# Optimization experiments

Hardware: AMD Instinct MI355X
Metric: run time of the kernel (lower is better)

Reference implementation:

```python
import jax, jax.numpy as jnp
import numpy as np

N = 50000      # nodes
E = 800000     # edges
F = 128        # num_features
DIM = 128      # dim
NF = 4         # n_factor
ND = DIM // NF # n_dim = 32
NL = 3         # n_layer
NC = 10        # n_class
G = 256        # num graphs in batch


def setup_inputs() -> dict:
    key = jax.random.key(0)
    ks = jax.random.split(key, 20)
    w = lambda k, shape, fan: (jax.random.normal(k, shape, jnp.float32) / np.sqrt(fan)).astype(jnp.float32)
    inp = {}
    inp["x"] = jax.random.normal(ks[0], (N, F), jnp.float32)
    inp["edge_index"] = jax.random.randint(ks[1], (2, E), 0, N)
    inp["batch"] = jnp.sort(jax.random.randint(ks[2], (N,), 0, G))
    # attention branch: lin0 (F->DIM) and att linear (2*DIM -> 1) per factor
    inp["lin0_W"] = w(ks[3], (NF, F, DIM), F)
    inp["lin0_b"] = jnp.zeros((NF, DIM), jnp.float32)
    inp["att_W"] = w(ks[4], (NF, 2 * DIM), 2 * DIM)
    inp["att_b"] = jnp.zeros((NF,), jnp.float32)
    # encoder per-factor input linear (F -> ND)
    inp["enc_W"] = w(ks[5], (NF, F, ND), F)
    inp["enc_b"] = jnp.zeros((NF, ND), jnp.float32)
    # GraphConv per factor/layer: lin_rel (with bias) + lin_root (no bias)
    inp["conv_Wrel"] = w(ks[6], (NF, NL, ND, ND), ND)
    inp["conv_brel"] = jnp.zeros((NF, NL, ND), jnp.float32)
    inp["conv_Wroot"] = w(ks[7], (NF, NL, ND, ND), ND)
    # GRU per factor (input ND, hidden ND), torch layout: [3*H, in]
    inp["gru_Wih"] = w(ks[8], (NF, 3 * ND, ND), ND)
    inp["gru_Whh"] = w(ks[9], (NF, 3 * ND, ND), ND)
    inp["gru_bih"] = jnp.zeros((NF, 3 * ND), jnp.float32)
    inp["gru_bhh"] = jnp.zeros((NF, 3 * ND), jnp.float32)
    # head
    inp["fc1_W"] = w(ks[10], (DIM, DIM), DIM)
    inp["fc1_b"] = jnp.zeros((DIM,), jnp.float32)
    inp["fc2_W"] = w(ks[11], (DIM, NC), DIM)
    inp["fc2_b"] = jnp.zeros((NC,), jnp.float32)
    return inp


def _gru_step(m, h, Wih, Whh, bih, bhh):
    # torch GRUCell math; gates order [r, z, n]
    gi = m @ Wih.T + bih   # [N, 3H]
    gh = h @ Whh.T + bhh
    ir, iz, inn = jnp.split(gi, 3, axis=-1)
    hr, hz, hn = jnp.split(gh, 3, axis=-1)
    r = jax.nn.sigmoid(ir + hr)
    z = jax.nn.sigmoid(iz + hz)
    n = jnp.tanh(inn + r * hn)
    return (1.0 - z) * n + z * h


def reference(x, edge_index, batch, lin0_W, lin0_b, att_W, att_b, enc_W, enc_b,
              conv_Wrel, conv_brel, conv_Wroot, gru_Wih, gru_Whh, gru_bih, gru_bhh,
              fc1_W, fc1_b, fc2_W, fc2_b):
    src, dst = edge_index[0], edge_index[1]
    counts = jnp.maximum(jax.ops.segment_sum(jnp.ones((N,), jnp.float32), batch, num_segments=G), 1.0)
    outs, atts = [], []
    for f in range(NF):
        # edge attention: sigmoid(6 * Linear([lin0(x[src]) || lin0(x[dst])]))
        a = x @ lin0_W[f] + lin0_b[f]                     # [N, DIM]
        Wl, Wr = att_W[f, :DIM], att_W[f, DIM:]
        e = a[src] @ Wl + a[dst] @ Wr + att_b[f]          # [E]
        att_i = jax.nn.sigmoid(6.0 * e)
        atts.append(att_i)
        # disentangled encoder for this factor
        out = x @ enc_W[f] + enc_b[f]                     # [N, ND]
        h = out
        for l in range(NL):
            # GraphConv: lin_rel(scatter_add(x[src]*w -> dst)) + lin_root(x)
            msg = out[src] * att_i[:, None]               # [E, ND]
            agg = jax.ops.segment_sum(msg, dst, num_segments=N)
            m = jax.nn.relu(agg @ conv_Wrel[f, l] + conv_brel[f, l] + out @ conv_Wroot[f, l])
            h = _gru_step(m, h, gru_Wih[f], gru_Whh[f], gru_bih[f], gru_bhh[f])
            out = h
        pooled = jax.ops.segment_sum(out, batch, num_segments=G) / counts[:, None]  # [G, ND]
        outs.append(pooled)
    out_cat = jnp.concatenate(outs, axis=-1)              # [G, DIM]
    pred = jax.nn.relu(out_cat @ fc1_W + fc1_b) @ fc2_W + fc2_b  # [G, NC]
    return pred, jnp.stack(atts, 0), jnp.stack(outs, 0)
```

## Files before the change

kernel.cpp:

```cpp
#include <hip/hip_runtime.h>
#include <hip/hip_fp16.h>
#include <math.h>

#define N   50000
#define E   800000
#define F   128
#define DIM 128
#define NF  4
#define ND  32
#define NL  3
#define NC  10
#define G   256
#define NB  196

typedef __attribute__((ext_vector_type(8))) short  s16x8;
typedef __attribute__((ext_vector_type(4))) float  f32x4;

__device__ __forceinline__ float sigm(float v) { return 1.0f / (1.0f + __expf(-v)); }

__device__ __forceinline__ unsigned int f2bf(float x) {
    unsigned int u = __float_as_uint(x);
    return (u + 0x7FFFu + ((u >> 16) & 1u)) >> 16;
}

__device__ __forceinline__ void split8(const float* v, s16x8& hi, s16x8& lo) {
    #pragma unroll
    for (int i = 0; i < 8; ++i) {
        float x = v[i];
        unsigned int h = f2bf(x);
        float hf = __uint_as_float(h << 16);
        hi[i] = (short)h;
        lo[i] = (short)f2bf(x - hf);
    }
}

#define MFMA(a, b, c) c = __builtin_amdgcn_mfma_f32_16x16x32_bf16(a, b, c, 0, 0, 0)
#define MF3(xh, xl, wh, wl, c) do { MFMA(xh, wh, c); MFMA(xh, wl, c); MFMA(xl, wh, c); } while (0)

__global__ void prep_kernel(const float* __restrict__ lin0_W, const float* __restrict__ lin0_b,
                            const float* __restrict__ att_W, const float* __restrict__ att_b,
                            float* __restrict__ vl, float* __restrict__ vr, float* __restrict__ cc) {
    int t = blockIdx.x * blockDim.x + threadIdx.x;
    if (t < NF * F) {
        int f = t >> 7, k = t & 127;
        const float* W  = lin0_W + (size_t)f * F * DIM + (size_t)k * DIM;
        const float* wl = att_W + f * 2 * DIM;
        const float* wr = wl + DIM;
        float sl = 0.f, sr = 0.f;
        for (int j = 0; j < DIM; ++j) { sl += W[j] * wl[j]; sr += W[j] * wr[j]; }
        vl[t] = sl; vr[t] = sr;
    }
    if (t < NF) {
        const float* b  = lin0_b + t * DIM;
        const float* wl = att_W + t * 2 * DIM;
        const float* wr = wl + DIM;
        float s = att_b[t];
        for (int j = 0; j < DIM; ++j) s += b[j] * (wl[j] + wr[j]);
        cc[t] = s;
    }
}

__global__ void wfrag_kernel(const float* __restrict__ Wrel, const float* __restrict__ Wroot,
                             const float* __restrict__ Wih, const float* __restrict__ Whh,
                             const float* __restrict__ enc_W,
                             const float* __restrict__ vl, const float* __restrict__ vr,
                             unsigned short* __restrict__ convfrag,
                             unsigned short* __restrict__ grufrag,
                             unsigned short* __restrict__ encfrag,
                             unsigned short* __restrict__ attfrag) {
    int b = blockIdx.x;
    int l = threadIdx.x;
    int lr = l & 15, lg = l >> 4;
    if (b < 12) {
        const float* wrelg  = Wrel  + (size_t)b * 1024;
        const float* wrootg = Wroot + (size_t)b * 1024;
        #pragma unroll
        for (int H = 0; H < 2; ++H) {
            #pragma unroll
            for (int i = 0; i < 8; ++i) {
                float x = wrelg[(lg * 8 + i) * 32 + H * 16 + lr];
                unsigned int h = f2bf(x);
                convfrag[(((size_t)b * 8 + 0 + H) * 64 + l) * 8 + i] = (unsigned short)h;
                convfrag[(((size_t)b * 8 + 2 + H) * 64 + l) * 8 + i] =
                    (unsigned short)f2bf(x - __uint_as_float(h << 16));
                x = wrootg[(lg * 8 + i) * 32 + H * 16 + lr];
                h = f2bf(x);
                convfrag[(((size_t)b * 8 + 4 + H) * 64 + l) * 8 + i] = (unsigned short)h;
                convfrag[(((size_t)b * 8 + 6 + H) * 64 + l) * 8 + i] =
                    (unsigned short)f2bf(x - __uint_as_float(h << 16));
            }
        }
    } else if (b < 16) {
        int f = b - 12;
        const float* wihg = Wih + (size_t)f * 3072;
        const float* whhg = Whh + (size_t)f * 3072;
        #pragma unroll
        for (int m = 0; m < 6; ++m) {
            const float* base = (m < 3 ? wihg : whhg) + (size_t)((m % 3) * 32) * 32;
            #pragma unroll
            for (int H = 0; H < 2; ++H) {
                int col = H * 16 + lr;
                #pragma unroll
                for (int i = 0; i < 8; ++i) {
                    float x = base[(size_t)col * 32 + lg * 8 + i];
                    unsigned int h = f2bf(x);
                    grufrag[(((size_t)(f * 6 + m) * 4 + H) * 64 + l) * 8 + i] = (unsigned short)h;
                    grufrag[(((size_t)(f * 6 + m) * 4 + 2 + H) * 64 + l) * 8 + i] =
                        (unsigned short)f2bf(x - __uint_as_float(h << 16));
                }
            }
        }
    } else {
        int f = b - 16;
        const float* we = enc_W + (size_t)f * F * ND;
        #pragma unroll
        for (int c = 0; c < 4; ++c) {
            #pragma unroll
            for (int i = 0; i < 8; ++i) {
                int k = c * 32 + lg * 8 + i;
                #pragma unroll
                for (int H = 0; H < 2; ++H) {
                    float x = we[(size_t)k * 32 + H * 16 + lr];
                    unsigned int h = f2bf(x);
                    encfrag[((((size_t)(f * 4 + c) * 2 + H) * 2 + 0) * 64 + l) * 8 + i] =
                        (unsigned short)h;
                    encfrag[((((size_t)(f * 4 + c) * 2 + H) * 2 + 1) * 64 + l) * 8 + i] =
                        (unsigned short)f2bf(x - __uint_as_float(h << 16));
                }
                float av = (lr == 0) ? vl[f * F + k] : (lr == 1) ? vr[f * F + k] : 0.f;
                unsigned int ha = f2bf(av);
                attfrag[(((size_t)(f * 4 + c) * 2 + 0) * 64 + l) * 8 + i] = (unsigned short)ha;
                attfrag[(((size_t)(f * 4 + c) * 2 + 1) * 64 + l) * 8 + i] =
                    (unsigned short)f2bf(av - __uint_as_float(ha << 16));
            }
        }
    }
}

__global__ __launch_bounds__(256) void encode_kernel(
        const float* __restrict__ x,
        const unsigned short* __restrict__ encfrag,
        const unsigned short* __restrict__ attfrag,
        const float* __restrict__ enc_b,
        float* __restrict__ out, unsigned short* __restrict__ st16,
        float* __restrict__ alr) {
    int tid = threadIdx.x;
    int f  = __builtin_amdgcn_readfirstlane(tid >> 6);
    int l  = tid & 63;
    int lr = l & 15, lg = l >> 4;
    int node0 = blockIdx.x * 32;

    s16x8 beh[4][2], bel[4][2], bah[4], bal[4];
    #pragma unroll
    for (int c = 0; c < 4; ++c) {
        #pragma unroll
        for (int H = 0; H < 2; ++H) {
            beh[c][H] = *(const s16x8*)&encfrag[((((size_t)(f*4 + c)*2 + H)*2 + 0)*64 + l)*8];
            bel[c][H] = *(const s16x8*)&encfrag[((((size_t)(f*4 + c)*2 + H)*2 + 1)*64 + l)*8];
        }
        bah[c] = *(const s16x8*)&attfrag[(((size_t)(f*4 + c)*2 + 0)*64 + l)*8];
        bal[c] = *(const s16x8*)&attfrag[(((size_t)(f*4 + c)*2 + 1)*64 + l)*8];
    }
    float be0 = enc_b[f*32 + lr], be1 = enc_b[f*32 + 16 + lr];

    #pragma unroll
    for (int s = 0; s < 2; ++s) {
        int n0 = node0 + s * 16;
        int na = n0 + lr; int nac = na < N ? na : N - 1;
        const float* px = x + (size_t)nac * F + lg * 8;
        s16x8 xh[4], xl[4];
        #pragma unroll
        for (int c = 0; c < 4; ++c) {
            float v[8];
            float4 q0 = *(const float4*)(px + c * 32);
            float4 q1 = *(const float4*)(px + c * 32 + 4);
            v[0]=q0.x; v[1]=q0.y; v[2]=q0.z; v[3]=q0.w; v[4]=q1.x; v[5]=q1.y; v[6]=q1.z; v[7]=q1.w;
            split8(v, xh[c], xl[c]);
        }
        f32x4 o0 = {be0, be0, be0, be0};
        f32x4 o1 = {be1, be1, be1, be1};
        f32x4 ca = {0.f, 0.f, 0.f, 0.f};
        #pragma unroll
        for (int c = 0; c < 4; ++c) {
            MF3(xh[c], xl[c], beh[c][0], bel[c][0], o0);
            MF3(xh[c], xl[c], beh[c][1], bel[c][1], o1);
            MF3(xh[c], xl[c], bah[c],    bal[c],    ca);
        }
        #pragma unroll
        for (int j = 0; j < 4; ++j) {
            int n = n0 + lg * 4 + j;
            if (n < N) {
                out[(size_t)n * DIM + f * ND + lr]       = o0[j];
                out[(size_t)n * DIM + f * ND + 16 + lr]  = o1[j];
                st16[(size_t)n * DIM + f * ND + lr]      = (unsigned short)f2bf(o0[j]);
                st16[(size_t)n * DIM + f * ND + 16 + lr] = (unsigned short)f2bf(o1[j]);
                if (lr == 0)      alr[(size_t)n * 8 + f]     = ca[j];
                else if (lr == 1) alr[(size_t)n * 8 + 4 + f] = ca[j];
            }
        }
    }
}

__global__ void hist_kernel(const int* __restrict__ ei, int* __restrict__ deg) {
    int e = blockIdx.x * 256 + threadIdx.x;
    if (e < E) atomicAdd(&deg[ei[E + e]], 1);
}

__global__ void scan1_kernel(const int* __restrict__ deg, int* __restrict__ rowp,
                             int* __restrict__ bsum) {
    __shared__ int sh[256];
    int i = blockIdx.x * 256 + threadIdx.x;
    int v = (i < N) ? deg[i] : 0;
    sh[threadIdx.x] = v;
    __syncthreads();
    for (int off = 1; off < 256; off <<= 1) {
        int t = 0;
        if ((int)threadIdx.x >= off) t = sh[threadIdx.x - off];
        __syncthreads();
        sh[threadIdx.x] += t;
        __syncthreads();
    }
    if (i < N) rowp[i] = sh[threadIdx.x] - v;
    if (threadIdx.x == 255) bsum[blockIdx.x] = sh[255];
}

__global__ void scan2_kernel(int* __restrict__ bsum) {
    __shared__ int sh[256];
    int v = ((int)threadIdx.x < NB) ? bsum[threadIdx.x] : 0;
    sh[threadIdx.x] = v;
    __syncthreads();
    for (int off = 1; off < 256; off <<= 1) {
        int t = 0;
        if ((int)threadIdx.x >= off) t = sh[threadIdx.x - off];
        __syncthreads();
        sh[threadIdx.x] += t;
        __syncthreads();
    }
    if ((int)threadIdx.x < NB) bsum[threadIdx.x] = sh[threadIdx.x] - v;
}

__global__ void scan3_kernel(int* __restrict__ rowp, const int* __restrict__ bsum) {
    int i = blockIdx.x * 256 + threadIdx.x;
    if (i < N) rowp[i] += bsum[i >> 8];
}

__global__ void fill_kernel(const int* __restrict__ ei, const float* __restrict__ alr,
                            const float* __restrict__ cc,
                            const int* __restrict__ rowp, int* __restrict__ cnt,
                            uint4* __restrict__ erec, float* __restrict__ atts) {
    int e = blockIdx.x * 256 + threadIdx.x;
    if (e >= E) return;
    int s = ei[e];
    int d = ei[E + e];
    float4 al = *(const float4*)(alr + (size_t)s * 8);
    float4 ar = *(const float4*)(alr + (size_t)d * 8 + 4);
    float a0 = sigm(6.f * (al.x + ar.x + cc[0]));
    float a1 = sigm(6.f * (al.y + ar.y + cc[1]));
    float a2 = sigm(6.f * (al.z + ar.z + cc[2]));
    float a3 = sigm(6.f * (al.w + ar.w + cc[3]));
    atts[e]                 = a0;
    atts[(size_t)E + e]     = a1;
    atts[2 * (size_t)E + e] = a2;
    atts[3 * (size_t)E + e] = a3;
    unsigned int p01 = (unsigned int)__half_as_ushort(__float2half(a0))
                     | ((unsigned int)__half_as_ushort(__float2half(a1)) << 16);
    unsigned int p23 = (unsigned int)__half_as_ushort(__float2half(a2))
                     | ((unsigned int)__half_as_ushort(__float2half(a3)) << 16);
    int slot = rowp[d] + atomicAdd(&cnt[d], 1);
    erec[slot] = make_uint4((unsigned int)s, p01, p23, 0u);
}

__global__ __launch_bounds__(256) void gather_kernel(
        const uint4* __restrict__ erec,
        const int* __restrict__ rowp, const int* __restrict__ deg,
        const unsigned short* __restrict__ st16,
        unsigned int* __restrict__ agghi, unsigned int* __restrict__ agglo) {
    int gw = (blockIdx.x << 2) | ((int)threadIdx.x >> 6);
    int n = __builtin_amdgcn_readfirstlane(gw);
    int lane = threadIdx.x & 63;
    int f = lane >> 4;
    int beg = rowp[n];
    int cnt = deg[n];
    const unsigned char* rp = (const unsigned char*)(erec + beg);
    const int aoff = 4 + (f >> 1) * 4;
    const int ash  = (f & 1) * 16;
    const unsigned short* ob = st16 + lane * 2;
    float ax = 0.f, ay = 0.f;
    int i = 0;
    #define RECS(k)  (*(const int*)(rp + (size_t)(i + k) * 16))
    #define RECA(k)  __half2float(__ushort_as_half((unsigned short)( \
                        (*(const unsigned int*)(rp + (size_t)(i + k) * 16 + aoff)) >> ash)))
    for (; i + 8 <= cnt; i += 8) {
        int s0 = RECS(0), s1 = RECS(1), s2 = RECS(2), s3 = RECS(3);
        int s4 = RECS(4), s5 = RECS(5), s6 = RECS(6), s7 = RECS(7);
        float a0 = RECA(0), a1 = RECA(1), a2 = RECA(2), a3 = RECA(3);
        float a4 = RECA(4), a5 = RECA(5), a6 = RECA(6), a7 = RECA(7);
        unsigned int u0 = *(const unsigned int*)(ob + (size_t)s0 * DIM);
        unsigned int u1 = *(const unsigned int*)(ob + (size_t)s1 * DIM);
        unsigned int u2 = *(const unsigned int*)(ob + (size_t)s2 * DIM);
        unsigned int u3 = *(const unsigned int*)(ob + (size_t)s3 * DIM);
        unsigned int u4 = *(const unsigned int*)(ob + (size_t)s4 * DIM);
        unsigned int u5 = *(const unsigned int*)(ob + (size_t)s5 * DIM);
        unsigned int u6 = *(const unsigned int*)(ob + (size_t)s6 * DIM);
        unsigned int u7 = *(const unsigned int*)(ob + (size_t)s7 * DIM);
        ax += a0 * __uint_as_float(u0 << 16) + a1 * __uint_as_float(u1 << 16)
            + a2 * __uint_as_float(u2 << 16) + a3 * __uint_as_float(u3 << 16)
            + a4 * __uint_as_float(u4 << 16) + a5 * __uint_as_float(u5 << 16)
            + a6 * __uint_as_float(u6 << 16) + a7 * __uint_as_float(u7 << 16);
        ay += a0 * __uint_as_float(u0 & 0xFFFF0000u) + a1 * __uint_as_float(u1 & 0xFFFF0000u)
            + a2 * __uint_as_float(u2 & 0xFFFF0000u) + a3 * __uint_as_float(u3 & 0xFFFF0000u)
            + a4 * __uint_as_float(u4 & 0xFFFF0000u) + a5 * __uint_as_float(u5 & 0xFFFF0000u)
            + a6 * __uint_as_float(u6 & 0xFFFF0000u) + a7 * __uint_as_float(u7 & 0xFFFF0000u);
    }
    for (; i + 4 <= cnt; i += 4) {
        int s0 = RECS(0), s1 = RECS(1), s2 = RECS(2), s3 = RECS(3);
        float a0 = RECA(0), a1 = RECA(1), a2 = RECA(2), a3 = RECA(3);
        unsigned int u0 = *(const unsigned int*)(ob + (size_t)s0 * DIM);
        unsigned int u1 = *(const unsigned int*)(ob + (size_t)s1 * DIM);
        unsigned int u2 = *(const unsigned int*)(ob + (size_t)s2 * DIM);
        unsigned int u3 = *(const unsigned int*)(ob + (size_t)s3 * DIM);
        ax += a0 * __uint_as_float(u0 << 16) + a1 * __uint_as_float(u1 << 16)
            + a2 * __uint_as_float(u2 << 16) + a3 * __uint_as_float(u3 << 16);
        ay += a0 * __uint_as_float(u0 & 0xFFFF0000u) + a1 * __uint_as_float(u1 & 0xFFFF0000u)
            + a2 * __uint_as_float(u2 & 0xFFFF0000u) + a3 * __uint_as_float(u3 & 0xFFFF0000u);
    }
    for (; i < cnt; ++i) {
        int s = RECS(0);
        float a = RECA(0);
        unsigned int u = *(const unsigned int*)(ob + (size_t)s * DIM);
        ax += a * __uint_as_float(u << 16);
        ay += a * __uint_as_float(u & 0xFFFF0000u);
    }
    #undef RECS
    #undef RECA
    unsigned int hx = f2bf(ax), hy = f2bf(ay);
    float fx = __uint_as_float(hx << 16), fy = __uint_as_float(hy << 16);
    agghi[(size_t)n * 64 + lane] = hx | (hy << 16);
    agglo[(size_t)n * 64 + lane] = f2bf(ax - fx) | (f2bf(ay - fy) << 16);
}

__global__ __launch_bounds__(256) void update_kernel(
        const unsigned int* __restrict__ agghi, const unsigned int* __restrict__ agglo,
        float* __restrict__ out, unsigned short* __restrict__ st16,
        const unsigned short* __restrict__ convfrag, const unsigned short* __restrict__ grufrag,
        const float* __restrict__ brel,
        const float* __restrict__ bih, const float* __restrict__ bhh, int lay) {
    __shared__ __align__(16) unsigned short mls[NF][2][2][16 * 40];
    int tid = threadIdx.x;
    int f   = __builtin_amdgcn_readfirstlane(tid >> 6);
    int l   = tid & 63;
    int lr  = l & 15;
    int lg  = l >> 4;
    int node0 = blockIdx.x * 32;

    const unsigned short* cf = convfrag + (size_t)(f * NL + lay) * 8 * 64 * 8;
    s16x8 wrelh[2], wrell[2], wrooth[2], wrootl[2];
    #pragma unroll
    for (int H = 0; H < 2; ++H) {
        wrelh[H]  = *(const s16x8*)&cf[((0 + H) * 64 + l) * 8];
        wrell[H]  = *(const s16x8*)&cf[((2 + H) * 64 + l) * 8];
        wrooth[H] = *(const s16x8*)&cf[((4 + H) * 64 + l) * 8];
        wrootl[H] = *(const s16x8*)&cf[((6 + H) * 64 + l) * 8];
    }
    const unsigned short* gf = grufrag + (size_t)f * 6 * 4 * 64 * 8;
    s16x8 wirh[2], wirl[2], wizh[2], wizl[2], winh[2], winl[2];
    s16x8 whrh[2], whrl[2], whzh[2], whzl[2], whnh[2], whnl[2];
    #pragma unroll
    for (int H = 0; H < 2; ++H) {
        wirh[H] = *(const s16x8*)&gf[((0 * 4 + H) * 64 + l) * 8];
        wirl[H] = *(const s16x8*)&gf[((0 * 4 + 2 + H) * 64 + l) * 8];
        wizh[H] = *(const s16x8*)&gf[((1 * 4 + H) * 64 + l) * 8];
        wizl[H] = *(const s16x8*)&gf[((1 * 4 + 2 + H) * 64 + l) * 8];
        winh[H] = *(const s16x8*)&gf[((2 * 4 + H) * 64 + l) * 8];
        winl[H] = *(const s16x8*)&gf[((2 * 4 + 2 + H) * 64 + l) * 8];
        whrh[H] = *(const s16x8*)&gf[((3 * 4 + H) * 64 + l) * 8];
        whrl[H] = *(const s16x8*)&gf[((3 * 4 + 2 + H) * 64 + l) * 8];
        whzh[H] = *(const s16x8*)&gf[((4 * 4 + H) * 64 + l) * 8];
        whzl[H] = *(const s16x8*)&gf[((4 * 4 + 2 + H) * 64 + l) * 8];
        whnh[H] = *(const s16x8*)&gf[((5 * 4 + H) * 64 + l) * 8];
        whnl[H] = *(const s16x8*)&gf[((5 * 4 + 2 + H) * 64 + l) * 8];
    }

    float br_[2], bir_[2], biz_[2], bin_[2], bhn_[2];
    #pragma unroll
    for (int H = 0; H < 2; ++H) {
        int c = H * 16 + lr;
        br_[H]  = brel[(f * NL + lay) * 32 + c];
        bir_[H] = bih[f * 96 + c]      + bhh[f * 96 + c];
        biz_[H] = bih[f * 96 + 32 + c] + bhh[f * 96 + 32 + c];
        bin_[H] = bih[f * 96 + 64 + c];
        bhn_[H] = bhh[f * 96 + 64 + c];
    }

    const unsigned short* ahp = (const unsigned short*)agghi;
    const unsigned short* alp = (const unsigned short*)agglo;

    #pragma unroll
    for (int s = 0; s < 2; ++s) {
        int n0 = node0 + s * 16;
        unsigned short* mHi = &mls[f][s][0][0];
        unsigned short* mLo = &mls[f][s][1][0];
        int na  = n0 + lr;
        int nac = na < N ? na : N - 1;
        s16x8 aggH = *(const s16x8*)&ahp[(size_t)nac * DIM + f * ND + lg * 8];
        s16x8 aggL = *(const s16x8*)&alp[(size_t)nac * DIM + f * ND + lg * 8];
        const float* ph = out + (size_t)nac * DIM + f * ND + lg * 8;
        float vh[8];
        { float4 q0 = *(const float4*)ph, q1 = *(const float4*)(ph + 4);
          vh[0]=q0.x; vh[1]=q0.y; vh[2]=q0.z; vh[3]=q0.w; vh[4]=q1.x; vh[5]=q1.y; vh[6]=q1.z; vh[7]=q1.w; }
        s16x8 hH, hL;
        split8(vh, hH, hL);
        float hj0[4], hj1[4];
        #pragma unroll
        for (int j = 0; j < 4; ++j) {
            int nn_ = n0 + lg * 4 + j;
            int nnc = nn_ < N ? nn_ : N - 1;
            hj0[j] = out[(size_t)nnc * DIM + f * ND + lr];
            hj1[j] = out[(size_t)nnc * DIM + f * ND + 16 + lr];
        }

        f32x4 c0 = {br_[0], br_[0], br_[0], br_[0]};
        f32x4 c1 = {br_[1], br_[1], br_[1], br_[1]};
        MF3(aggH, aggL, wrelh[0],  wrell[0],  c0);
        MF3(hH,   hL,   wrooth[0], wrootl[0], c0);
        MF3(aggH, aggL, wrelh[1],  wrell[1],  c1);
        MF3(hH,   hL,   wrooth[1], wrootl[1], c1);

        #pragma unroll
        for (int j = 0; j < 4; ++j) {
            int row = lg * 4 + j;
            float v0 = fmaxf(c0[j], 0.f);
            float v1 = fmaxf(c1[j], 0.f);
            unsigned int h0 = f2bf(v0);
            unsigned int h1 = f2bf(v1);
            mHi[row * 40 + lr]      = (unsigned short)h0;
            mHi[row * 40 + 16 + lr] = (unsigned short)h1;
            mLo[row * 40 + lr]      = (unsigned short)f2bf(v0 - __uint_as_float(h0 << 16));
            mLo[row * 40 + 16 + lr] = (unsigned short)f2bf(v1 - __uint_as_float(h1 << 16));
        }
        __asm__ volatile("s_waitcnt lgkmcnt(0)" ::: "memory");
        __builtin_amdgcn_sched_barrier(0x37);
        s16x8 mH = *(const s16x8*)&mHi[lr * 40 + lg * 8];
        s16x8 mL = *(const s16x8*)&mLo[lr * 40 + lg * 8];

        f32x4 gr0 = {bir_[0], bir_[0], bir_[0], bir_[0]};
        f32x4 gr1 = {bir_[1], bir_[1], bir_[1], bir_[1]};
        f32x4 gz0 = {biz_[0], biz_[0], biz_[0], biz_[0]};
        f32x4 gz1 = {biz_[1], biz_[1], biz_[1], biz_[1]};
        f32x4 gn0 = {bin_[0], bin_[0], bin_[0], bin_[0]};
        f32x4 gn1 = {bin_[1], bin_[1], bin_[1], bin_[1]};
        f32x4 gh0 = {bhn_[0], bhn_[0], bhn_[0], bhn_[0]};
        f32x4 gh1 = {bhn_[1], bhn_[1], bhn_[1], bhn_[1]};
        MF3(mH, mL, wirh[0], wirl[0], gr0);  MF3(hH, hL, whrh[0], whrl[0], gr0);
        MF3(mH, mL, wirh[1], wirl[1], gr1);  MF3(hH, hL, whrh[1], whrl[1], gr1);
        MF3(mH, mL, wizh[0], wizl[0], gz0);  MF3(hH, hL, whzh[0], whzl[0], gz0);
        MF3(mH, mL, wizh[1], wizl[1], gz1);  MF3(hH, hL, whzh[1], whzl[1], gz1);
        MF3(mH, mL, winh[0], winl[0], gn0);
        MF3(mH, mL, winh[1], winl[1], gn1);
        MF3(hH, hL, whnh[0], whnl[0], gh0);
        MF3(hH, hL, whnh[1], whnl[1], gh1);

        #pragma unroll
        for (int j = 0; j < 4; ++j) {
            int n = n0 + lg * 4 + j;
            float r0 = sigm(gr0[j]);
            float z0 = sigm(gz0[j]);
            float t0 = 2.f * sigm(2.f * (gn0[j] + r0 * gh0[j])) - 1.f;
            float res0 = (1.f - z0) * t0 + z0 * hj0[j];
            float r1 = sigm(gr1[j]);
            float z1 = sigm(gz1[j]);
            float t1 = 2.f * sigm(2.f * (gn1[j] + r1 * gh1[j])) - 1.f;
            float res1 = (1.f - z1) * t1 + z1 * hj1[j];
            if (n < N) {
                out[(size_t)n * DIM + f * ND + lr]       = res0;
                out[(size_t)n * DIM + f * ND + 16 + lr]  = res1;
                st16[(size_t)n * DIM + f * ND + lr]      = (unsigned short)f2bf(res0);
                st16[(size_t)n * DIM + f * ND + 16 + lr] = (unsigned short)f2bf(res1);
            }
        }
    }
}

__global__ void goff_kernel(const int* __restrict__ batch, int* __restrict__ goff) {
    int g = threadIdx.x;
    int lo = 0, hi = N;
    while (lo < hi) {
        int mid = (lo + hi) >> 1;
        if (batch[mid] < g) lo = mid + 1; else hi = mid;
    }
    goff[g] = lo;
    if (g == 0) goff[G] = N;
}

__global__ void pool_kernel(const float* __restrict__ st, const int* __restrict__ goff,
                            float* __restrict__ pooled, float* __restrict__ outsout) {
    __shared__ float acc2[128];
    int g = blockIdx.x;
    int c = threadIdx.x & 127;
    int half = threadIdx.x >> 7;
    int beg = goff[g], cnt = goff[g + 1] - beg;
    float acc = 0.f;
    for (int i = half; i < cnt; i += 2) acc += st[(size_t)(beg + i) * DIM + c];
    if (half == 1) acc2[c] = acc;
    __syncthreads();
    if (half == 0) {
        float tot = acc + acc2[c];
        float val = tot / fmaxf((float)cnt, 1.0f);
        pooled[g * DIM + c] = val;
        int f = c >> 5, d = c & 31;
        outsout[((size_t)f * G + g) * ND + d] = val;
    }
}

__global__ void mlp_kernel(const float* __restrict__ pooled,
                           const float* __restrict__ fc1_W, const float* __restrict__ fc1_b,
                           const float* __restrict__ fc2_W, const float* __restrict__ fc2_b,
                           float* __restrict__ pred) {
    __shared__ float row[DIM], hid[DIM];
    int g = blockIdx.x, c = threadIdx.x;
    row[c] = pooled[(size_t)g * DIM + c];
    __syncthreads();
    float acc = fc1_b[c];
    #pragma unroll 8
    for (int k = 0; k < DIM; ++k) acc += row[k] * fc1_W[k * DIM + c];
    hid[c] = fmaxf(acc, 0.f);
    __syncthreads();
    if (c < NC) {
        float p = fc2_b[c];
        for (int k = 0; k < DIM; ++k) p += hid[k] * fc2_W[k * NC + c];
        pred[(size_t)g * NC + c] = p;
    }
}

extern "C" void kernel_launch(void* const* d_in, const int* in_sizes, int n_in,
                              void* d_out, int out_size, void* d_ws, size_t ws_size,
                              hipStream_t stream) {
    const float* x         = (const float*)d_in[0];
    const int*   ei        = (const int*)  d_in[1];
    const int*   batch     = (const int*)  d_in[2];
    const float* lin0_W    = (const float*)d_in[3];
    const float* lin0_b    = (const float*)d_in[4];
    const float* att_W     = (const float*)d_in[5];
    const float* att_b     = (const float*)d_in[6];
    const float* enc_W     = (const float*)d_in[7];
    const float* enc_b     = (const float*)d_in[8];
    const float* conv_Wrel = (const float*)d_in[9];
    const float* conv_brel = (const float*)d_in[10];
    const float* conv_Wroot= (const float*)d_in[11];
    const float* gru_Wih   = (const float*)d_in[12];
    const float* gru_Whh   = (const float*)d_in[13];
    const float* gru_bih   = (const float*)d_in[14];
    const float* gru_bhh   = (const float*)d_in[15];
    const float* fc1_W     = (const float*)d_in[16];
    const float* fc1_b     = (const float*)d_in[17];
    const float* fc2_W     = (const float*)d_in[18];
    const float* fc2_b     = (const float*)d_in[19];

    float* outp    = (float*)d_out;
    float* pred    = outp;
    float* atts    = outp + G * NC;
    float* outsout = atts + (size_t)NF * E;

    float* fp     = (float*)d_ws;
    float* st     = fp;                   fp += (size_t)N * DIM;
    unsigned int* agghi = (unsigned int*)fp;     fp += (size_t)N * 64;
    unsigned int* agglo = (unsigned int*)fp;     fp += (size_t)N * 64;
    unsigned short* st16 = (unsigned short*)fp;  fp += (size_t)N * DIM / 2;
    float* alr    = fp;                   fp += (size_t)N * 8;
    float* vl     = fp;                   fp += NF * F;
    float* vr     = fp;                   fp += NF * F;
    float* cc     = fp;                   fp += 4;
    float* pooled = fp;                   fp += G * DIM;
    unsigned short* convfrag = (unsigned short*)fp;  fp += 12 * 8 * 64 * 8 / 2;
    unsigned short* grufrag  = (unsigned short*)fp;  fp += 4 * 24 * 64 * 8 / 2;
    unsigned short* encfrag  = (unsigned short*)fp;  fp += 4 * 16 * 64 * 8 / 2;
    unsigned short* attfrag  = (unsigned short*)fp;  fp += 4 * 8 * 64 * 8 / 2;
    uint4* erec  = (uint4*)fp;            fp += (size_t)NF * E;
    int* ip    = (int*)fp;
    int* deg   = ip;                      ip += N;
    int* cnt   = ip;                      ip += N;
    int* rowp  = ip;                      ip += N;
    int* bsum  = ip;                      ip += 256;
    int* goff  = ip;                      ip += G + 1;

    hipMemsetAsync(deg, 0, (size_t)(2 * N) * sizeof(int), stream);

    prep_kernel<<<2, 256, 0, stream>>>(lin0_W, lin0_b, att_W, att_b, vl, vr, cc);
    wfrag_kernel<<<20, 64, 0, stream>>>(conv_Wrel, conv_Wroot, gru_Wih, gru_Whh,
                                        enc_W, vl, vr,
                                        convfrag, grufrag, encfrag, attfrag);
    goff_kernel<<<1, 256, 0, stream>>>(batch, goff);
    encode_kernel<<<(N + 31) / 32, 256, 0, stream>>>(x, encfrag, attfrag, enc_b,
                                                     st, st16, alr);

    hist_kernel<<<(E + 255) / 256, 256, 0, stream>>>(ei, deg);
    scan1_kernel<<<NB, 256, 0, stream>>>(deg, rowp, bsum);
    scan2_kernel<<<1, 256, 0, stream>>>(bsum);
    scan3_kernel<<<NB, 256, 0, stream>>>(rowp, bsum);
    fill_kernel<<<(E + 255) / 256, 256, 0, stream>>>(ei, alr, cc, rowp, cnt, erec, atts);

    for (int l = 0; l < NL; ++l) {
        gather_kernel<<<N / 4, 256, 0, stream>>>(erec, rowp, deg, st16, agghi, agglo);
        update_kernel<<<(N + 31) / 32, 256, 0, stream>>>(agghi, agglo, st, st16,
                                                         convfrag, grufrag, conv_brel,
                                                         gru_bih, gru_bhh, l);
    }

    pool_kernel<<<G, 256, 0, stream>>>(st, goff, pooled, outsout);
    mlp_kernel<<<G, DIM, 0, stream>>>(pooled, fc1_W, fc1_b, fc2_W, fc2_b, pred);
}
```

Before: 475.2 us.

## Compact edge records to 16-bit sources and recompute attention in gather

Edge records shrink from 16-byte uint4 (source plus fp16 attention weights) to a 16-bit source index. The attention sigmoid is recomputed in the gather kernel from per-node alr values, so less edge data is written and re-read each layer. The fp32 node state buffer is also replaced by a hi/lo bf16 pair, so the update kernel reads split fragments directly instead of re-splitting fp32. The 16-bit source index only works because N fits in 65536. Recomputing attention per edge per lane adds an extra gathered alr load and an exp per edge.

```diff
diff --git a/kernel.cpp b/kernel.cpp
--- a/kernel.cpp
+++ b/kernel.cpp
@@ -22,6 +22,8 @@
     unsigned int u = __float_as_uint(x);
     return (u + 0x7FFFu + ((u >> 16) & 1u)) >> 16;
 }
+
+__device__ __forceinline__ float bfval(unsigned int h) { return __uint_as_float(h << 16); }
 
 __device__ __forceinline__ void split8(const float* v, s16x8& hi, s16x8& lo) {
     #pragma unroll
@@ -142,7 +144,7 @@
         const unsigned short* __restrict__ encfrag,
         const unsigned short* __restrict__ attfrag,
         const float* __restrict__ enc_b,
-        float* __restrict__ out, unsigned short* __restrict__ st16,
+        unsigned short* __restrict__ st16, unsigned short* __restrict__ stlo,
         float* __restrict__ alr) {
     int tid = threadIdx.x;
     int f  = __builtin_amdgcn_readfirstlane(tid >> 6);
@@ -190,10 +192,12 @@
         for (int j = 0; j < 4; ++j) {
             int n = n0 + lg * 4 + j;
             if (n < N) {
-                out[(size_t)n * DIM + f * ND + lr]       = o0[j];
-                out[(size_t)n * DIM + f * ND + 16 + lr]  = o1[j];
-                st16[(size_t)n * DIM + f * ND + lr]      = (unsigned short)f2bf(o0[j]);
-                st16[(size_t)n * DIM + f * ND + 16 + lr] = (unsigned short)f2bf(o1[j]);
+                unsigned int h0 = f2bf(o0[j]);
+                unsigned int h1 = f2bf(o1[j]);
+                st16[(size_t)n * DIM + f * ND + lr]       = (unsigned short)h0;
+                st16[(size_t)n * DIM + f * ND + 16 + lr]  = (unsigned short)h1;
+                stlo[(size_t)n * DIM + f * ND + lr]       = (unsigned short)f2bf(o0[j] - bfval(h0));
+                stlo[(size_t)n * DIM + f * ND + 16 + lr]  = (unsigned short)f2bf(o1[j] - bfval(h1));
                 if (lr == 0)      alr[(size_t)n * 8 + f]     = ca[j];
                 else if (lr == 1) alr[(size_t)n * 8 + 4 + f] = ca[j];
             }
@@ -247,7 +251,7 @@
 __global__ void fill_kernel(const int* __restrict__ ei, const float* __restrict__ alr,
                             const float* __restrict__ cc,
                             const int* __restrict__ rowp, int* __restrict__ cnt,
-                            uint4* __restrict__ erec, float* __restrict__ atts) {
+                            unsigned short* __restrict__ esrc, float* __restrict__ atts) {
     int e = blockIdx.x * 256 + threadIdx.x;
     if (e >= E) return;
     int s = ei[e];
@@ -262,18 +266,15 @@
     atts[(size_t)E + e]     = a1;
     atts[2 * (size_t)E + e] = a2;
     atts[3 * (size_t)E + e] = a3;
-    unsigned int p01 = (unsigned int)__half_as_ushort(__float2half(a0))
-                     | ((unsigned int)__half_as_ushort(__float2half(a1)) << 16);
-    unsigned int p23 = (unsigned int)__half_as_ushort(__float2half(a2))
-                     | ((unsigned int)__half_as_ushort(__float2half(a3)) << 16);
     int slot = rowp[d] + atomicAdd(&cnt[d], 1);
-    erec[slot] = make_uint4((unsigned int)s, p01, p23, 0u);
+    esrc[slot] = (unsigned short)s;
 }
 
 __global__ __launch_bounds__(256) void gather_kernel(
-        const uint4* __restrict__ erec,
+        const unsigned short* __restrict__ esrc,
         const int* __restrict__ rowp, const int* __restrict__ deg,
         const unsigned short* __restrict__ st16,
+        const float* __restrict__ alr, const float* __restrict__ cc,
         unsigned int* __restrict__ agghi, unsigned int* __restrict__ agglo) {
     int gw = (blockIdx.x << 2) | ((int)threadIdx.x >> 6);
     int n = __builtin_amdgcn_readfirstlane(gw);
@@ -281,20 +282,18 @@
     int f = lane >> 4;
     int beg = rowp[n];
     int cnt = deg[n];
-    const unsigned char* rp = (const unsigned char*)(erec + beg);
-    const int aoff = 4 + (f >> 1) * 4;
-    const int ash  = (f & 1) * 16;
+    const unsigned short* sp = esrc + beg;
+    const float* alf = alr + f;
+    float arc = alr[(size_t)n * 8 + 4 + f] + cc[f];
     const unsigned short* ob = st16 + lane * 2;
     float ax = 0.f, ay = 0.f;
     int i = 0;
-    #define RECS(k)  (*(const int*)(rp + (size_t)(i + k) * 16))
-    #define RECA(k)  __half2float(__ushort_as_half((unsigned short)( \
-                        (*(const unsigned int*)(rp + (size_t)(i + k) * 16 + aoff)) >> ash)))
+    #define ATT(sv) sigm(6.f * (alf[(size_t)(sv) * 8] + arc))
     for (; i + 8 <= cnt; i += 8) {
-        int s0 = RECS(0), s1 = RECS(1), s2 = RECS(2), s3 = RECS(3);
-        int s4 = RECS(4), s5 = RECS(5), s6 = RECS(6), s7 = RECS(7);
-        float a0 = RECA(0), a1 = RECA(1), a2 = RECA(2), a3 = RECA(3);
-        float a4 = RECA(4), a5 = RECA(5), a6 = RECA(6), a7 = RECA(7);
+        int s0 = sp[i],     s1 = sp[i + 1], s2 = sp[i + 2], s3 = sp[i + 3];
+        int s4 = sp[i + 4], s5 = sp[i + 5], s6 = sp[i + 6], s7 = sp[i + 7];
+        float a0 = ATT(s0), a1 = ATT(s1), a2 = ATT(s2), a3 = ATT(s3);
+        float a4 = ATT(s4), a5 = ATT(s5), a6 = ATT(s6), a7 = ATT(s7);
         unsigned int u0 = *(const unsigned int*)(ob + (size_t)s0 * DIM);
         unsigned int u1 = *(const unsigned int*)(ob + (size_t)s1 * DIM);
         unsigned int u2 = *(const unsigned int*)(ob + (size_t)s2 * DIM);
@@ -313,8 +312,8 @@
             + a6 * __uint_as_float(u6 & 0xFFFF0000u) + a7 * __uint_as_float(u7 & 0xFFFF0000u);
     }
     for (; i + 4 <= cnt; i += 4) {
-        int s0 = RECS(0), s1 = RECS(1), s2 = RECS(2), s3 = RECS(3);
-        float a0 = RECA(0), a1 = RECA(1), a2 = RECA(2), a3 = RECA(3);
+        int s0 = sp[i], s1 = sp[i + 1], s2 = sp[i + 2], s3 = sp[i + 3];
+        float a0 = ATT(s0), a1 = ATT(s1), a2 = ATT(s2), a3 = ATT(s3);
         unsigned int u0 = *(const unsigned int*)(ob + (size_t)s0 * DIM);
         unsigned int u1 = *(const unsigned int*)(ob + (size_t)s1 * DIM);
         unsigned int u2 = *(const unsigned int*)(ob + (size_t)s2 * DIM);
@@ -325,14 +324,13 @@
             + a2 * __uint_as_float(u2 & 0xFFFF0000u) + a3 * __uint_as_float(u3 & 0xFFFF0000u);
     }
     for (; i < cnt; ++i) {
-        int s = RECS(0);
-        float a = RECA(0);
+        int s = sp[i];
+        float a = ATT(s);
         unsigned int u = *(const unsigned int*)(ob + (size_t)s * DIM);
         ax += a * __uint_as_float(u << 16);
         ay += a * __uint_as_float(u & 0xFFFF0000u);
     }
-    #undef RECS
-    #undef RECA
+    #undef ATT
     unsigned int hx = f2bf(ax), hy = f2bf(ay);
     float fx = __uint_as_float(hx << 16), fy = __uint_as_float(hy << 16);
     agghi[(size_t)n * 64 + lane] = hx | (hy << 16);
@@ -341,7 +339,7 @@
 
 __global__ __launch_bounds__(256) void update_kernel(
         const unsigned int* __restrict__ agghi, const unsigned int* __restrict__ agglo,
-        float* __restrict__ out, unsigned short* __restrict__ st16,
+        unsigned short* __restrict__ st16, unsigned short* __restrict__ stlo,
         const unsigned short* __restrict__ convfrag, const unsigned short* __restrict__ grufrag,
         const float* __restrict__ brel,
         const float* __restrict__ bih, const float* __restrict__ bhh, int lay) {
@@ -404,19 +402,16 @@
         int nac = na < N ? na : N - 1;
         s16x8 aggH = *(const s16x8*)&ahp[(size_t)nac * DIM + f * ND + lg * 8];
         s16x8 aggL = *(const s16x8*)&alp[(size_t)nac * DIM + f * ND + lg * 8];
-        const float* ph = out + (size_t)nac * DIM + f * ND + lg * 8;
-        float vh[8];
-        { float4 q0 = *(const float4*)ph, q1 = *(const float4*)(ph + 4);
-          vh[0]=q0.x; vh[1]=q0.y; vh[2]=q0.z; vh[3]=q0.w; vh[4]=q1.x; vh[5]=q1.y; vh[6]=q1.z; vh[7]=q1.w; }
-        s16x8 hH, hL;
-        split8(vh, hH, hL);
+        s16x8 hH   = *(const s16x8*)&st16[(size_t)nac * DIM + f * ND + lg * 8];
+        s16x8 hL   = *(const s16x8*)&stlo[(size_t)nac * DIM + f * ND + lg * 8];
         float hj0[4], hj1[4];
         #pragma unroll
         for (int j = 0; j < 4; ++j) {
             int nn_ = n0 + lg * 4 + j;
             int nnc = nn_ < N ? nn_ : N - 1;
-            hj0[j] = out[(size_t)nnc * DIM + f * ND + lr];
-            hj1[j] = out[(size_t)nnc * DIM + f * ND + 16 + lr];
+            size_t b0 = (size_t)nnc * DIM + f * ND + lr;
+            hj0[j] = bfval(st16[b0])      + bfval(stlo[b0]);
+            hj1[j] = bfval(st16[b0 + 16]) + bfval(stlo[b0 + 16]);
         }
 
         f32x4 c0 = {br_[0], br_[0], br_[0], br_[0]};
@@ -472,10 +467,13 @@
             float t1 = 2.f * sigm(2.f * (gn1[j] + r1 * gh1[j])) - 1.f;
             float res1 = (1.f - z1) * t1 + z1 * hj1[j];
             if (n < N) {
-                out[(size_t)n * DIM + f * ND + lr]       = res0;
-                out[(size_t)n * DIM + f * ND + 16 + lr]  = res1;
-                st16[(size_t)n * DIM + f * ND + lr]      = (unsigned short)f2bf(res0);
-                st16[(size_t)n * DIM + f * ND + 16 + lr] = (unsigned short)f2bf(res1);
+                size_t b0 = (size_t)n * DIM + f * ND + lr;
+                unsigned int h0 = f2bf(res0);
+                unsigned int h1 = f2bf(res1);
+                st16[b0]      = (unsigned short)h0;
+                st16[b0 + 16] = (unsigned short)h1;
+                stlo[b0]      = (unsigned short)f2bf(res0 - bfval(h0));
+                stlo[b0 + 16] = (unsigned short)f2bf(res1 - bfval(h1));
             }
         }
     }
@@ -492,7 +490,9 @@
     if (g == 0) goff[G] = N;
 }
 
-__global__ void pool_kernel(const float* __restrict__ st, const int* __restrict__ goff,
+__global__ void pool_kernel(const unsigned short* __restrict__ st16,
+                            const unsigned short* __restrict__ stlo,
+                            const int* __restrict__ goff,
                             float* __restrict__ pooled, float* __restrict__ outsout) {
     __shared__ float acc2[128];
     int g = blockIdx.x;
@@ -500,7 +500,10 @@
     int half = threadIdx.x >> 7;
     int beg = goff[g], cnt = goff[g + 1] - beg;
     float acc = 0.f;
-    for (int i = half; i < cnt; i += 2) acc += st[(size_t)(beg + i) * DIM + c];
+    for (int i = half; i < cnt; i += 2) {
+        size_t idx = (size_t)(beg + i) * DIM + c;
+        acc += bfval(st16[idx]) + bfval(stlo[idx]);
+    }
     if (half == 1) acc2[c] = acc;
     __syncthreads();
     if (half == 0) {
@@ -562,10 +565,10 @@
     float* outsout = atts + (size_t)NF * E;
 
     float* fp     = (float*)d_ws;
-    float* st     = fp;                   fp += (size_t)N * DIM;
     unsigned int* agghi = (unsigned int*)fp;     fp += (size_t)N * 64;
     unsigned int* agglo = (unsigned int*)fp;     fp += (size_t)N * 64;
     unsigned short* st16 = (unsigned short*)fp;  fp += (size_t)N * DIM / 2;
+    unsigned short* stlo = (unsigned short*)fp;  fp += (size_t)N * DIM / 2;
     float* alr    = fp;                   fp += (size_t)N * 8;
     float* vl     = fp;                   fp += NF * F;
     float* vr     = fp;                   fp += NF * F;
@@ -575,7 +578,7 @@
     unsigned short* grufrag  = (unsigned short*)fp;  fp += 4 * 24 * 64 * 8 / 2;
     unsigned short* encfrag  = (unsigned short*)fp;  fp += 4 * 16 * 64 * 8 / 2;
     unsigned short* attfrag  = (unsigned short*)fp;  fp += 4 * 8 * 64 * 8 / 2;
-    uint4* erec  = (uint4*)fp;            fp += (size_t)NF * E;
+    unsigned short* esrc = (unsigned short*)fp;  fp += E / 2 + 4;
     int* ip    = (int*)fp;
     int* deg   = ip;                      ip += N;
     int* cnt   = ip;                      ip += N;
@@ -591,21 +594,22 @@
                                         convfrag, grufrag, encfrag, attfrag);
     goff_kernel<<<1, 256, 0, stream>>>(batch, goff);
     encode_kernel<<<(N + 31) / 32, 256, 0, stream>>>(x, encfrag, attfrag, enc_b,
-                                                     st, st16, alr);
+                                                     st16, stlo, alr);
 
     hist_kernel<<<(E + 255) / 256, 256, 0, stream>>>(ei, deg);
     scan1_kernel<<<NB, 256, 0, stream>>>(deg, rowp, bsum);
     scan2_kernel<<<1, 256, 0, stream>>>(bsum);
     scan3_kernel<<<NB, 256, 0, stream>>>(rowp, bsum);
-    fill_kernel<<<(E + 255) / 256, 256, 0, stream>>>(ei, alr, cc, rowp, cnt, erec, atts);
+    fill_kernel<<<(E + 255) / 256, 256, 0, stream>>>(ei, alr, cc, rowp, cnt, esrc, atts);
 
     for (int l = 0; l < NL; ++l) {
-        gather_kernel<<<N / 4, 256, 0, stream>>>(erec, rowp, deg, st16, agghi, agglo);
-        update_kernel<<<(N + 31) / 32, 256, 0, stream>>>(agghi, agglo, st, st16,
+        gather_kernel<<<N / 4, 256, 0, stream>>>(esrc, rowp, deg, st16, alr, cc,
+                                                 agghi, agglo);
+        update_kernel<<<(N + 31) / 32, 256, 0, stream>>>(agghi, agglo, st16, stlo,
                                                          convfrag, grufrag, conv_brel,
                                                          gru_bih, gru_bhh, l);
     }
 
-    pool_kernel<<<G, 256, 0, stream>>>(st, goff, pooled, outsout);
+    pool_kernel<<<G, 256, 0, stream>>>(st16, stlo, goff, pooled, outsout);
     mlp_kernel<<<G, DIM, 0, stream>>>(pooled, fc1_W, fc1_b, fc2_W, fc2_b, pred);
 }
```

Result: slower. 538.2 us (+13.3%).

## Fuse neighbor gather into GRU update kernel with ping-pong state buffers

Applied to the files above, without the earlier changes.

Merges the per-layer gather and update kernels into one kernel. Each block first gathers the attention-weighted neighbor sums for its 32 nodes into shared memory, then runs the MFMA conv and GRU math on them. This removes the global round trip of the aggregation buffers and one launch per layer. Because all blocks must read the previous state while others write the new one, the state arrays now alternate between two buffers. The cost is that the gather now runs with 16 lanes per node across 8 node rows per wave, which may expose less memory parallelism than the old one-wave-per-node gather. The unroll depth also drops from 8 to 4.

```diff
diff --git a/kernel.cpp b/kernel.cpp
--- a/kernel.cpp
+++ b/kernel.cpp
@@ -22,6 +22,8 @@
     unsigned int u = __float_as_uint(x);
     return (u + 0x7FFFu + ((u >> 16) & 1u)) >> 16;
 }
+
+__device__ __forceinline__ float bfval(unsigned int h) { return __uint_as_float(h << 16); }
 
 __device__ __forceinline__ void split8(const float* v, s16x8& hi, s16x8& lo) {
     #pragma unroll
@@ -270,88 +272,77 @@
     erec[slot] = make_uint4((unsigned int)s, p01, p23, 0u);
 }
 
-__global__ __launch_bounds__(256) void gather_kernel(
+__global__ __launch_bounds__(256) void gupdate_kernel(
         const uint4* __restrict__ erec,
         const int* __restrict__ rowp, const int* __restrict__ deg,
-        const unsigned short* __restrict__ st16,
-        unsigned int* __restrict__ agghi, unsigned int* __restrict__ agglo) {
-    int gw = (blockIdx.x << 2) | ((int)threadIdx.x >> 6);
-    int n = __builtin_amdgcn_readfirstlane(gw);
-    int lane = threadIdx.x & 63;
-    int f = lane >> 4;
-    int beg = rowp[n];
-    int cnt = deg[n];
-    const unsigned char* rp = (const unsigned char*)(erec + beg);
-    const int aoff = 4 + (f >> 1) * 4;
-    const int ash  = (f & 1) * 16;
-    const unsigned short* ob = st16 + lane * 2;
-    float ax = 0.f, ay = 0.f;
-    int i = 0;
-    #define RECS(k)  (*(const int*)(rp + (size_t)(i + k) * 16))
-    #define RECA(k)  __half2float(__ushort_as_half((unsigned short)( \
-                        (*(const unsigned int*)(rp + (size_t)(i + k) * 16 + aoff)) >> ash)))
-    for (; i + 8 <= cnt; i += 8) {
-        int s0 = RECS(0), s1 = RECS(1), s2 = RECS(2), s3 = RECS(3);
-        int s4 = RECS(4), s5 = RECS(5), s6 = RECS(6), s7 = RECS(7);
-        float a0 = RECA(0), a1 = RECA(1), a2 = RECA(2), a3 = RECA(3);
-        float a4 = RECA(4), a5 = RECA(5), a6 = RECA(6), a7 = RECA(7);
-        unsigned int u0 = *(const unsigned int*)(ob + (size_t)s0 * DIM);
-        unsigned int u1 = *(const unsigned int*)(ob + (size_t)s1 * DIM);
-        unsigned int u2 = *(const unsigned int*)(ob + (size_t)s2 * DIM);
-        unsigned int u3 = *(const unsigned int*)(ob + (size_t)s3 * DIM);
-        unsigned int u4 = *(const unsigned int*)(ob + (size_t)s4 * DIM);
-        unsigned int u5 = *(const unsigned int*)(ob + (size_t)s5 * DIM);
-        unsigned int u6 = *(const unsigned int*)(ob + (size_t)s6 * DIM);
-        unsigned int u7 = *(const unsigned int*)(ob + (size_t)s7 * DIM);
-        ax += a0 * __uint_as_float(u0 << 16) + a1 * __uint_as_float(u1 << 16)
-            + a2 * __uint_as_float(u2 << 16) + a3 * __uint_as_float(u3 << 16)
-            + a4 * __uint_as_float(u4 << 16) + a5 * __uint_as_float(u5 << 16)
-            + a6 * __uint_as_float(u6 << 16) + a7 * __uint_as_float(u7 << 16);
-        ay += a0 * __uint_as_float(u0 & 0xFFFF0000u) + a1 * __uint_as_float(u1 & 0xFFFF0000u)
-            + a2 * __uint_as_float(u2 & 0xFFFF0000u) + a3 * __uint_as_float(u3 & 0xFFFF0000u)
-            + a4 * __uint_as_float(u4 & 0xFFFF0000u) + a5 * __uint_as_float(u5 & 0xFFFF0000u)
-            + a6 * __uint_as_float(u6 & 0xFFFF0000u) + a7 * __uint_as_float(u7 & 0xFFFF0000u);
-    }
-    for (; i + 4 <= cnt; i += 4) {
-        int s0 = RECS(0), s1 = RECS(1), s2 = RECS(2), s3 = RECS(3);
-        float a0 = RECA(0), a1 = RECA(1), a2 = RECA(2), a3 = RECA(3);
-        unsigned int u0 = *(const unsigned int*)(ob + (size_t)s0 * DIM);
-        unsigned int u1 = *(const unsigned int*)(ob + (size_t)s1 * DIM);
-        unsigned int u2 = *(const unsigned int*)(ob + (size_t)s2 * DIM);
-        unsigned int u3 = *(const unsigned int*)(ob + (size_t)s3 * DIM);
-        ax += a0 * __uint_as_float(u0 << 16) + a1 * __uint_as_float(u1 << 16)
-            + a2 * __uint_as_float(u2 << 16) + a3 * __uint_as_float(u3 << 16);
-        ay += a0 * __uint_as_float(u0 & 0xFFFF0000u) + a1 * __uint_as_float(u1 & 0xFFFF0000u)
-            + a2 * __uint_as_float(u2 & 0xFFFF0000u) + a3 * __uint_as_float(u3 & 0xFFFF0000u);
-    }
-    for (; i < cnt; ++i) {
-        int s = RECS(0);
-        float a = RECA(0);
-        unsigned int u = *(const unsigned int*)(ob + (size_t)s * DIM);
-        ax += a * __uint_as_float(u << 16);
-        ay += a * __uint_as_float(u & 0xFFFF0000u);
-    }
-    #undef RECS
-    #undef RECA
-    unsigned int hx = f2bf(ax), hy = f2bf(ay);
-    float fx = __uint_as_float(hx << 16), fy = __uint_as_float(hy << 16);
-    agghi[(size_t)n * 64 + lane] = hx | (hy << 16);
-    agglo[(size_t)n * 64 + lane] = f2bf(ax - fx) | (f2bf(ay - fy) << 16);
-}
-
-__global__ __launch_bounds__(256) void update_kernel(
-        const unsigned int* __restrict__ agghi, const unsigned int* __restrict__ agglo,
-        float* __restrict__ out, unsigned short* __restrict__ st16,
+        const float* __restrict__ outin, const unsigned short* __restrict__ st16in,
+        float* __restrict__ outout, unsigned short* __restrict__ st16out,
         const unsigned short* __restrict__ convfrag, const unsigned short* __restrict__ grufrag,
         const float* __restrict__ brel,
         const float* __restrict__ bih, const float* __restrict__ bhh, int lay) {
     __shared__ __align__(16) unsigned short mls[NF][2][2][16 * 40];
+    __shared__ __align__(16) unsigned int  aggls[NF][2][2][16 * 20];
     int tid = threadIdx.x;
     int f   = __builtin_amdgcn_readfirstlane(tid >> 6);
     int l   = tid & 63;
     int lr  = l & 15;
     int lg  = l >> 4;
     int node0 = blockIdx.x * 32;
+
+    {
+        int g = l >> 4;
+        int c = l & 15;
+        const int aoff = 4 + (f >> 1) * 4;
+        const int ash  = (f & 1) * 16;
+        const unsigned short* op = st16in + f * ND + c * 2;
+        for (int r = 0; r < 8; ++r) {
+            int node = r * 4 + g;
+            int n = node0 + node;
+            int nc2 = n < N ? n : N - 1;
+            int beg = rowp[nc2];
+            int cnt = deg[nc2];
+            const unsigned char* rp8 = (const unsigned char*)(erec + beg);
+            float ax = 0.f, ay = 0.f;
+            int i = 0;
+            for (; i + 4 <= cnt; i += 4) {
+                unsigned int s0 = *(const unsigned int*)(rp8 + (size_t)(i + 0) * 16);
+                unsigned int s1 = *(const unsigned int*)(rp8 + (size_t)(i + 1) * 16);
+                unsigned int s2 = *(const unsigned int*)(rp8 + (size_t)(i + 2) * 16);
+                unsigned int s3 = *(const unsigned int*)(rp8 + (size_t)(i + 3) * 16);
+                float a0 = __half2float(__ushort_as_half((unsigned short)(
+                    (*(const unsigned int*)(rp8 + (size_t)(i + 0) * 16 + aoff)) >> ash)));
+                float a1 = __half2float(__ushort_as_half((unsigned short)(
+                    (*(const unsigned int*)(rp8 + (size_t)(i + 1) * 16 + aoff)) >> ash)));
+                float a2 = __half2float(__ushort_as_half((unsigned short)(
+                    (*(const unsigned int*)(rp8 + (size_t)(i + 2) * 16 + aoff)) >> ash)));
+                float a3 = __half2float(__ushort_as_half((unsigned short)(
+                    (*(const unsigned int*)(rp8 + (size_t)(i + 3) * 16 + aoff)) >> ash)));
+                unsigned int u0 = *(const unsigned int*)(op + (size_t)s0 * DIM);
+                unsigned int u1 = *(const unsigned int*)(op + (size_t)s1 * DIM);
+                unsigned int u2 = *(const unsigned int*)(op + (size_t)s2 * DIM);
+                unsigned int u3 = *(const unsigned int*)(op + (size_t)s3 * DIM);
+                ax += a0 * __uint_as_float(u0 << 16) + a1 * __uint_as_float(u1 << 16)
+                    + a2 * __uint_as_float(u2 << 16) + a3 * __uint_as_float(u3 << 16);
+                ay += a0 * __uint_as_float(u0 & 0xFFFF0000u) + a1 * __uint_as_float(u1 & 0xFFFF0000u)
+                    + a2 * __uint_as_float(u2 & 0xFFFF0000u) + a3 * __uint_as_float(u3 & 0xFFFF0000u);
+            }
+            for (; i < cnt; ++i) {
+                unsigned int s = *(const unsigned int*)(rp8 + (size_t)i * 16);
+                float a = __half2float(__ushort_as_half((unsigned short)(
+                    (*(const unsigned int*)(rp8 + (size_t)i * 16 + aoff)) >> ash)));
+                unsigned int u = *(const unsigned int*)(op + (size_t)s * DIM);
+                ax += a * __uint_as_float(u << 16);
+                ay += a * __uint_as_float(u & 0xFFFF0000u);
+            }
+            int sub = node >> 4, row = node & 15;
+            unsigned int hx = f2bf(ax), hy = f2bf(ay);
+            aggls[f][sub][0][row * 20 + c] = hx | (hy << 16);
+            aggls[f][sub][1][row * 20 + c] =
+                f2bf(ax - bfval(hx)) | (f2bf(ay - bfval(hy)) << 16);
+        }
+    }
+    __asm__ volatile("s_waitcnt lgkmcnt(0)" ::: "memory");
+    __builtin_amdgcn_sched_barrier(0);
 
     const unsigned short* cf = convfrag + (size_t)(f * NL + lay) * 8 * 64 * 8;
     s16x8 wrelh[2], wrell[2], wrooth[2], wrootl[2];
@@ -392,19 +383,16 @@
         bhn_[H] = bhh[f * 96 + 64 + c];
     }
 
-    const unsigned short* ahp = (const unsigned short*)agghi;
-    const unsigned short* alp = (const unsigned short*)agglo;
-
     #pragma unroll
     for (int s = 0; s < 2; ++s) {
         int n0 = node0 + s * 16;
         unsigned short* mHi = &mls[f][s][0][0];
         unsigned short* mLo = &mls[f][s][1][0];
+        s16x8 aggH = *(const s16x8*)((const unsigned short*)&aggls[f][s][0][0] + lr * 40 + lg * 8);
+        s16x8 aggL = *(const s16x8*)((const unsigned short*)&aggls[f][s][1][0] + lr * 40 + lg * 8);
         int na  = n0 + lr;
         int nac = na < N ? na : N - 1;
-        s16x8 aggH = *(const s16x8*)&ahp[(size_t)nac * DIM + f * ND + lg * 8];
-        s16x8 aggL = *(const s16x8*)&alp[(size_t)nac * DIM + f * ND + lg * 8];
-        const float* ph = out + (size_t)nac * DIM + f * ND + lg * 8;
+        const float* ph = outin + (size_t)nac * DIM + f * ND + lg * 8;
         float vh[8];
         { float4 q0 = *(const float4*)ph, q1 = *(const float4*)(ph + 4);
           vh[0]=q0.x; vh[1]=q0.y; vh[2]=q0.z; vh[3]=q0.w; vh[4]=q1.x; vh[5]=q1.y; vh[6]=q1.z; vh[7]=q1.w; }
@@ -415,8 +403,8 @@
         for (int j = 0; j < 4; ++j) {
             int nn_ = n0 + lg * 4 + j;
             int nnc = nn_ < N ? nn_ : N - 1;
-            hj0[j] = out[(size_t)nnc * DIM + f * ND + lr];
-            hj1[j] = out[(size_t)nnc * DIM + f * ND + 16 + lr];
+            hj0[j] = outin[(size_t)nnc * DIM + f * ND + lr];
+            hj1[j] = outin[(size_t)nnc * DIM + f * ND + 16 + lr];
         }
 
         f32x4 c0 = {br_[0], br_[0], br_[0], br_[0]};
@@ -472,10 +460,10 @@
             float t1 = 2.f * sigm(2.f * (gn1[j] + r1 * gh1[j])) - 1.f;
             float res1 = (1.f - z1) * t1 + z1 * hj1[j];
             if (n < N) {
-                out[(size_t)n * DIM + f * ND + lr]       = res0;
-                out[(size_t)n * DIM + f * ND + 16 + lr]  = res1;
-                st16[(size_t)n * DIM + f * ND + lr]      = (unsigned short)f2bf(res0);
-                st16[(size_t)n * DIM + f * ND + 16 + lr] = (unsigned short)f2bf(res1);
+                outout[(size_t)n * DIM + f * ND + lr]       = res0;
+                outout[(size_t)n * DIM + f * ND + 16 + lr]  = res1;
+                st16out[(size_t)n * DIM + f * ND + lr]      = (unsigned short)f2bf(res0);
+                st16out[(size_t)n * DIM + f * ND + 16 + lr] = (unsigned short)f2bf(res1);
             }
         }
     }
@@ -562,10 +550,10 @@
     float* outsout = atts + (size_t)NF * E;
 
     float* fp     = (float*)d_ws;
-    float* st     = fp;                   fp += (size_t)N * DIM;
-    unsigned int* agghi = (unsigned int*)fp;     fp += (size_t)N * 64;
-    unsigned int* agglo = (unsigned int*)fp;     fp += (size_t)N * 64;
-    unsigned short* st16 = (unsigned short*)fp;  fp += (size_t)N * DIM / 2;
+    float* out0   = fp;                   fp += (size_t)N * DIM;
+    float* out1   = fp;                   fp += (size_t)N * DIM;
+    unsigned short* st0 = (unsigned short*)fp;   fp += (size_t)N * DIM / 2;
+    unsigned short* st1 = (unsigned short*)fp;   fp += (size_t)N * DIM / 2;
     float* alr    = fp;                   fp += (size_t)N * 8;
     float* vl     = fp;                   fp += NF * F;
     float* vr     = fp;                   fp += NF * F;
@@ -591,7 +579,7 @@
                                         convfrag, grufrag, encfrag, attfrag);
     goff_kernel<<<1, 256, 0, stream>>>(batch, goff);
     encode_kernel<<<(N + 31) / 32, 256, 0, stream>>>(x, encfrag, attfrag, enc_b,
-                                                     st, st16, alr);
+                                                     out0, st0, alr);
 
     hist_kernel<<<(E + 255) / 256, 256, 0, stream>>>(ei, deg);
     scan1_kernel<<<NB, 256, 0, stream>>>(deg, rowp, bsum);
@@ -599,13 +587,17 @@
     scan3_kernel<<<NB, 256, 0, stream>>>(rowp, bsum);
     fill_kernel<<<(E + 255) / 256, 256, 0, stream>>>(ei, alr, cc, rowp, cnt, erec, atts);
 
-    for (int l = 0; l < NL; ++l) {
-        gather_kernel<<<N / 4, 256, 0, stream>>>(erec, rowp, deg, st16, agghi, agglo);
-        update_kernel<<<(N + 31) / 32, 256, 0, stream>>>(agghi, agglo, st, st16,
-                                                         convfrag, grufrag, conv_brel,
-                                                         gru_bih, gru_bhh, l);
-    }
-
-    pool_kernel<<<G, 256, 0, stream>>>(st, goff, pooled, outsout);
+    const float* oin = out0; const unsigned short* sin = st0;
+    float* oout = out1; unsigned short* sout = st1;
+    for (int lyr = 0; lyr < NL; ++lyr) {
+        gupdate_kernel<<<(N + 31) / 32, 256, 0, stream>>>(erec, rowp, deg,
+                                                          oin, sin, oout, sout,
+                                                          convfrag, grufrag, conv_brel,
+                                                          gru_bih, gru_bhh, lyr);
+        const float* to = oin; oin = oout; oout = (float*)to;
+        const unsigned short* ts = sin; sin = sout; sout = (unsigned short*)ts;
+    }
+
+    pool_kernel<<<G, 256, 0, stream>>>(oin, goff, pooled, outsout);
     mlp_kernel<<<G, DIM, 0, stream>>>(pooled, fc1_W, fc1_b, fc2_W, fc2_b, pred);
 }
```

Measured after the change: 754.6 us. +58.8%, slower.
